# Kernel optimization log

Hardware: AMD Instinct MI355X
Metric: run time of the kernel (lower is better)

The kernel has to match this reference:

```python
import jax, jax.numpy as jnp
import numpy as np

D_MODEL = 1024
NUM_HEADS = 16
D_K = D_MODEL // NUM_HEADS


def setup_inputs() -> dict:
    key = jax.random.key(0)
    ks = jax.random.split(key, 12)
    B, S = 2, 2048
    s = 1.0 / np.sqrt(D_MODEL)
    inp = {
        "query": jax.random.normal(ks[0], (B, S, D_MODEL), jnp.float32),
        "key": jax.random.normal(ks[1], (B, S, D_MODEL), jnp.float32),
        "value": jax.random.normal(ks[2], (B, S, D_MODEL), jnp.float32),
        "w_q": jax.random.normal(ks[3], (D_MODEL, D_MODEL), jnp.float32) * s,
        "b_q": jax.random.normal(ks[4], (D_MODEL,), jnp.float32) * 0.01,
        "w_k": jax.random.normal(ks[5], (D_MODEL, D_MODEL), jnp.float32) * s,
        "b_k": jax.random.normal(ks[6], (D_MODEL,), jnp.float32) * 0.01,
        "w_v": jax.random.normal(ks[7], (D_MODEL, D_MODEL), jnp.float32) * s,
        "b_v": jax.random.normal(ks[8], (D_MODEL,), jnp.float32) * 0.01,
        "w_o": jax.random.normal(ks[9], (D_MODEL, D_MODEL), jnp.float32) * s,
        "b_o": jax.random.normal(ks[10], (D_MODEL,), jnp.float32) * 0.01,
    }
    return inp


def _split_heads(x):
    # [B, S, d_model] -> [B, H, S, d_k]
    B, S, _ = x.shape
    return x.reshape(B, S, NUM_HEADS, D_K).transpose(0, 2, 1, 3)


def reference(query, key, value, w_q, b_q, w_k, b_k, w_v, b_v, w_o, b_o):
    B, S, _ = query.shape
    Q = _split_heads(query @ w_q.T + b_q)
    K = _split_heads(key @ w_k.T + b_k)
    V = _split_heads(value @ w_v.T + b_v)
    scale = 1.0 / jnp.sqrt(jnp.asarray(D_K, Q.dtype))
    scores = jnp.einsum("bhqd,bhkd->bhqk", Q, K) * scale  # [B,H,S,S]
    attn = jax.nn.softmax(scores, axis=-1)
    ctx = jnp.einsum("bhqk,bhkd->bhqd", attn, V)
    ctx = ctx.transpose(0, 2, 1, 3).reshape(B, S, D_MODEL)
    return ctx @ w_o.T + b_o
```

## Files before the change

kernel.cpp:

```cpp
#include <hip/hip_runtime.h>
#include <hip/hip_bf16.h>
#include <stdint.h>

#define D_MODEL 1024
#define NHEAD   16
#define DK      64
#define SEQ     2048
#define BATCH   2

using bf16 = __bf16;
typedef __bf16 bf16x8 __attribute__((ext_vector_type(8)));
typedef float  f32x4  __attribute__((ext_vector_type(4)));
typedef float  f32x16 __attribute__((ext_vector_type(16)));
typedef unsigned uintx2 __attribute__((ext_vector_type(2)));

__device__ __forceinline__ unsigned short f2bf(float x) {
  return __builtin_bit_cast(unsigned short, (__bf16)x);
}
__device__ __forceinline__ unsigned pk2bf(float a, float b) {
  return (unsigned)f2bf(a) | ((unsigned)f2bf(b) << 16);
}
__device__ __forceinline__ float uasf(unsigned x) {
  return __builtin_bit_cast(float, x);
}
__device__ __forceinline__ unsigned fasu(float x) {
  return __builtin_bit_cast(unsigned, x);
}

__device__ __forceinline__ void gld_lds16(const void* g, void* l) {
  __builtin_amdgcn_global_load_lds(
      (const __attribute__((address_space(1))) void*)g,
      (__attribute__((address_space(3))) void*)l, 16, 0, 0);
}

__device__ __forceinline__ float xhalf_sum(float x) {
  uintx2 r = __builtin_amdgcn_permlane32_swap(fasu(x), fasu(x), false, false);
  return uasf(r[0]) + uasf(r[1]);
}

#define MHA_PACK(sv, off, dst)                                           \
  {                                                                      \
    float e0 = __builtin_amdgcn_exp2f(sv[off + 0]);                      \
    float e1 = __builtin_amdgcn_exp2f(sv[off + 1]);                      \
    float e2 = __builtin_amdgcn_exp2f(sv[off + 2]);                      \
    float e3 = __builtin_amdgcn_exp2f(sv[off + 3]);                      \
    float e4 = __builtin_amdgcn_exp2f(sv[off + 4]);                      \
    float e5 = __builtin_amdgcn_exp2f(sv[off + 5]);                      \
    float e6 = __builtin_amdgcn_exp2f(sv[off + 6]);                      \
    float e7 = __builtin_amdgcn_exp2f(sv[off + 7]);                      \
    ps += ((e0 + e1) + (e2 + e3)) + ((e4 + e5) + (e6 + e7));             \
    unsigned c0 = pk2bf(e0, e1), c1 = pk2bf(e2, e3);                     \
    unsigned c2 = pk2bf(e4, e5), c3 = pk2bf(e6, e7);                     \
    uintx2 r02 = __builtin_amdgcn_permlane32_swap(c0, c2, false, false); \
    uintx2 r13 = __builtin_amdgcn_permlane32_swap(c1, c3, false, false); \
    uint4 w; w.x = r02[0]; w.y = r13[0]; w.z = r02[1]; w.w = r13[1];     \
    dst = __builtin_bit_cast(bf16x8, w);                                 \
  }

struct ConvArgs {
  const float* src[7];
  bf16* dst[7];
};

__global__ __launch_bounds__(256) void convert_f32_bf16(ConvArgs a) {
  int v = blockIdx.x * 256 + threadIdx.x;
  int seg, off;
  if (v < 3 * 1048576) { seg = v >> 20; off = v & (1048576 - 1); }
  else { int u = v - 3 * 1048576; seg = 3 + (u >> 18); off = u & (262144 - 1); }
  float4 f = ((const float4*)a.src[seg])[off];
  ushort4 o;
  o.x = f2bf(f.x); o.y = f2bf(f.y); o.z = f2bf(f.z); o.w = f2bf(f.w);
  ((ushort4*)a.dst[seg])[off] = o;
}

__device__ __forceinline__ void gemm_qkv_core(
    const bf16* __restrict__ A, const bf16* __restrict__ B,
    const float* __restrict__ bias, bf16* __restrict__ Cout,
    int mode, int bx, int by, float oscale, char* lds) {
  constexpr int BUF = 16384;
  constexpr int NKT = D_MODEL / 32;
  const int tid  = threadIdx.x;
  const int lane = tid & 63;
  const int wave = tid >> 6;
  const int wr = wave >> 1, wc = wave & 1;
  const int t = lane >> 4, q = lane & 15;

  f32x4 acc[4][4];
#pragma unroll
  for (int i = 0; i < 4; ++i)
#pragma unroll
    for (int j = 0; j < 4; ++j) acc[i][j] = (f32x4){0.f, 0.f, 0.f, 0.f};

  const char* Abase = (const char*)(A + (size_t)bx * 128 * D_MODEL);
  const char* Bbase = (const char*)(B + (size_t)by * 128 * D_MODEL);

  const char* gA[2]; char* sA[2]; const char* gB[2]; char* sB[2];
#pragma unroll
  for (int i = 0; i < 2; ++i) {
    int c = tid + i * 256, row = c >> 2;
    int src = ((c & 3) * 16) ^ ((row & 3) << 4);
    gA[i] = Abase + (size_t)row * (D_MODEL * 2) + src;
    sA[i] = lds + c * 16;
    gB[i] = Bbase + (size_t)row * (D_MODEL * 2) + src;
    sB[i] = lds + 8192 + c * 16;
  }

  const char* aA[4]; const char* aB[4];
#pragma unroll
  for (int f = 0; f < 4; ++f) {
    int ra = wr * 64 + f * 16 + q;
    aA[f] = lds + ra * 64 + ((t * 16) ^ ((q & 3) << 4));
    int rb = wc * 64 + f * 16 + q;
    aB[f] = lds + 8192 + rb * 64 + ((t * 16) ^ ((q & 3) << 4));
  }

#pragma unroll
  for (int i = 0; i < 2; ++i) { gld_lds16(gA[i], sA[i]); gld_lds16(gB[i], sB[i]); }
#pragma unroll
  for (int i = 0; i < 2; ++i) {
    gld_lds16(gA[i] + 64, sA[i] + BUF); gld_lds16(gB[i] + 64, sB[i] + BUF);
  }
  asm volatile("s_waitcnt vmcnt(4)" ::: "memory");
  __builtin_amdgcn_s_barrier();

#pragma unroll
  for (int kt = 0; kt < NKT; ++kt) {
    const int CUR = (kt % 3) * BUF;
    if (kt + 2 < NKT) {
      const int NB = ((kt + 2) % 3) * BUF;
#pragma unroll
      for (int i = 0; i < 2; ++i) {
        gld_lds16(gA[i] + (kt + 2) * 64, sA[i] + NB);
        gld_lds16(gB[i] + (kt + 2) * 64, sB[i] + NB);
      }
    }
    bf16x8 af[4], bfv[4];
#pragma unroll
    for (int f = 0; f < 4; ++f) af[f]  = *(const bf16x8*)(aA[f] + CUR);
#pragma unroll
    for (int f = 0; f < 4; ++f) bfv[f] = *(const bf16x8*)(aB[f] + CUR);
    __builtin_amdgcn_s_setprio(1);
#pragma unroll
    for (int fm = 0; fm < 4; ++fm)
#pragma unroll
      for (int fn = 0; fn < 4; ++fn)
        acc[fm][fn] = __builtin_amdgcn_mfma_f32_16x16x32_bf16(
            af[fm], bfv[fn], acc[fm][fn], 0, 0, 0);
    __builtin_amdgcn_s_setprio(0);
    if (kt + 2 < NKT)      asm volatile("s_waitcnt vmcnt(4)" ::: "memory");
    else if (kt + 1 < NKT) asm volatile("s_waitcnt vmcnt(0)" ::: "memory");
    __builtin_amdgcn_s_barrier();
  }

#pragma unroll
  for (int fm = 0; fm < 4; ++fm)
#pragma unroll
    for (int fn = 0; fn < 4; ++fn)
#pragma unroll
      for (int jj = 0; jj < 4; ++jj) {
        int m = bx * 128 + wr * 64 + fm * 16 + t * 4 + jj;
        int n = by * 128 + wc * 64 + fn * 16 + q;
        float v = acc[fm][fn][jj];
        if (mode == 0) {
          v = (v + bias[n]) * oscale;
          int b = m >> 11, s = m & (SEQ - 1), h = n >> 6, d = n & 63;
          Cout[(((size_t)(b * NHEAD + h)) * SEQ + s) * DK + d] = (bf16)v;
        } else {
          v += bias[m];
          int h = m >> 6, d = m & 63, b = n >> 11, s = n & (SEQ - 1);
          Cout[(((size_t)(b * NHEAD + h)) * DK + d) * SEQ + s] = (bf16)v;
        }
      }
}

struct QkvArgs {
  const bf16* A[3]; const bf16* B[3]; const float* bias[3]; bf16* out[3];
};

__global__ __launch_bounds__(256, 2) void gemm_qkv(QkvArgs a) {
  __shared__ char lds[3 * 16384];
  int z = blockIdx.z;
  int mode = (z == 2) ? 1 : 0;
  int bx = (z == 2) ? blockIdx.y : blockIdx.x;
  int by = (z == 2) ? blockIdx.x : blockIdx.y;
  float osc = (z == 0) ? 0.18033688011112042f : 1.0f;
  gemm_qkv_core(a.A[z], a.B[z], a.bias[z], a.out[z], mode, bx, by, osc, lds);
}

template <int BM>
__device__ __forceinline__ void gemm_core(
    const bf16* __restrict__ A, const bf16* __restrict__ B,
    const float* __restrict__ bias, float* __restrict__ Cout,
    int bx, int by, char* lds) {
  constexpr int FM   = BM / 32;
  constexpr int ACH  = BM / 32;
  constexpr int HALF = BM * 128 + 16384;
  const int tid  = threadIdx.x;
  const int lane = tid & 63;
  const int wave = tid >> 6;
  const int wr = wave >> 1, wc = wave & 1;
  const int t = lane >> 4, q = lane & 15;

  f32x4 acc[FM][4];
#pragma unroll
  for (int i = 0; i < FM; ++i)
#pragma unroll
    for (int j = 0; j < 4; ++j) acc[i][j] = (f32x4){0.f, 0.f, 0.f, 0.f};

  const char* Abase = (const char*)(A + (size_t)bx * BM * D_MODEL);
  const char* Bbase = (const char*)(B + (size_t)by * 128 * D_MODEL);

  const char* gA[ACH]; char* sA[ACH];
  const char* gB[4];   char* sB[4];
#pragma unroll
  for (int i = 0; i < ACH; ++i) {
    int c = tid + i * 256, row = c >> 3;
    int src = ((c & 7) * 16) ^ ((row & 7) << 4);
    gA[i] = Abase + (size_t)row * (D_MODEL * 2) + src;
    sA[i] = lds + c * 16;
  }
#pragma unroll
  for (int i = 0; i < 4; ++i) {
    int c = tid + i * 256, row = c >> 3;
    int src = ((c & 7) * 16) ^ ((row & 7) << 4);
    gB[i] = Bbase + (size_t)row * (D_MODEL * 2) + src;
    sB[i] = lds + BM * 128 + c * 16;
  }

  const char* aA[FM][2]; const char* aB[4][2];
#pragma unroll
  for (int f = 0; f < FM; ++f)
#pragma unroll
    for (int ks = 0; ks < 2; ++ks) {
      int ra = wr * (BM / 2) + f * 16 + q;
      aA[f][ks] = lds + ra * 128 + ((ks * 64 + t * 16) ^ ((q & 7) << 4));
    }
#pragma unroll
  for (int f = 0; f < 4; ++f)
#pragma unroll
    for (int ks = 0; ks < 2; ++ks) {
      int rb = wc * 64 + f * 16 + q;
      aB[f][ks] = lds + BM * 128 + rb * 128 + ((ks * 64 + t * 16) ^ ((q & 7) << 4));
    }

#pragma unroll
  for (int i = 0; i < ACH; ++i) gld_lds16(gA[i], sA[i]);
#pragma unroll
  for (int i = 0; i < 4; ++i)  gld_lds16(gB[i], sB[i]);
  __syncthreads();

  auto ktile = [&](int kt, int CUR) {
    if (kt + 1 < D_MODEL / 64) {
      int NXT = CUR ^ HALF;
#pragma unroll
      for (int i = 0; i < ACH; ++i) gld_lds16(gA[i] + (kt + 1) * 128, sA[i] + NXT);
#pragma unroll
      for (int i = 0; i < 4; ++i)  gld_lds16(gB[i] + (kt + 1) * 128, sB[i] + NXT);
    }
#pragma unroll
    for (int ks = 0; ks < 2; ++ks) {
      bf16x8 af[FM], bfv[4];
#pragma unroll
      for (int f = 0; f < FM; ++f) af[f] = *(const bf16x8*)(aA[f][ks] + CUR);
#pragma unroll
      for (int f = 0; f < 4; ++f)  bfv[f] = *(const bf16x8*)(aB[f][ks] + CUR);
      __builtin_amdgcn_s_setprio(1);
#pragma unroll
      for (int fm = 0; fm < FM; ++fm)
#pragma unroll
        for (int fn = 0; fn < 4; ++fn)
          acc[fm][fn] = __builtin_amdgcn_mfma_f32_16x16x32_bf16(
              af[fm], bfv[fn], acc[fm][fn], 0, 0, 0);
      __builtin_amdgcn_s_setprio(0);
    }
    __syncthreads();
  };
  for (int kt = 0; kt < D_MODEL / 64; kt += 2) {
    ktile(kt, 0);
    ktile(kt + 1, HALF);
  }

#pragma unroll
  for (int fm = 0; fm < FM; ++fm)
#pragma unroll
    for (int fn = 0; fn < 4; ++fn)
#pragma unroll
      for (int jj = 0; jj < 4; ++jj) {
        int m = bx * BM + wr * (BM / 2) + fm * 16 + t * 4 + jj;
        int n = by * 128 + wc * 64 + fn * 16 + q;
        Cout[(size_t)m * D_MODEL + n] = acc[fm][fn][jj] + bias[n];
      }
}

__global__ __launch_bounds__(256, 2) void gemm_o(
    const bf16* __restrict__ A, const bf16* __restrict__ B,
    const float* __restrict__ bias, float* __restrict__ Cout) {
  __shared__ char lds[2 * (64 * 128 + 16384)];
  gemm_core<64>(A, B, bias, Cout, blockIdx.x, blockIdx.y, lds);
}

__global__ __launch_bounds__(512, 2) void flash_attn(
    const bf16* __restrict__ Qh, const bf16* __restrict__ Kh,
    const bf16* __restrict__ Vt, bf16* __restrict__ ctx) {
  __shared__ char lds[65536];
  const int tid  = threadIdx.x;
  const int lane = tid & 63;
  const int wave = tid >> 6;
  const int lo = lane & 31;
  const int hi = lane >> 5;
  const int grp = wave >> 2;
  const int wq  = wave & 3;
  const int bh = blockIdx.x;
  const int q0 = blockIdx.y * 128 + wq * 32;

  const bf16* Qb = Qh + (size_t)bh * SEQ * DK;
  const char* Kb = (const char*)(Kh + (size_t)bh * SEQ * DK) + grp * 1024 * 128;
  const char* Vb = (const char*)(Vt + (size_t)bh * DK * SEQ) + grp * 1024 * 2;
  char* Kg = lds + grp * 16384;
  char* Vg = lds + 32768 + grp * 16384;

  bf16x8 qf[4];
#pragma unroll
  for (int c = 0; c < 4; ++c)
    qf[c] = *(const bf16x8*)(Qb + (size_t)(q0 + lo) * DK + c * 16 + hi * 8);

  const int tg = tid & 255;
  const int srow = tg >> 3;
  const int ssrc = ((tg & 7) * 16) ^ ((srow & 7) << 4);
  const char* gK0 = Kb + (size_t)srow * 128 + ssrc;
  const char* gK1 = Kb + (size_t)(srow + 32) * 128 + ssrc;
  const char* gV0 = Vb + (size_t)srow * 4096 + ssrc;
  const char* gV1 = Vb + (size_t)(srow + 32) * 4096 + ssrc;
  char* sK0 = Kg + tg * 16;
  char* sK1 = Kg + 4096 + tg * 16;
  char* sV0 = Vg + tg * 16;
  char* sV1 = Vg + 4096 + tg * 16;

  const int key = (lo & 7) << 4;
  const char* KA[4]; const char* VA[4];
#pragma unroll
  for (int c = 0; c < 4; ++c) {
    int o = (((2 * c + hi) * 16) ^ key) + lo * 128;
    KA[c] = Kg + o;
    VA[c] = Vg + o;
  }

  f32x16 acc0 = {}, acc1 = {};
  float lsum = 0.f;

  gld_lds16(gK0, sK0); gld_lds16(gK1, sK1);
  gld_lds16(gV0, sV0); gld_lds16(gV1, sV1);
  __syncthreads();

  auto tile = [&](int kt, int CUR) {
    if (kt + 1 < 16) {
      int nb = CUR ^ 8192;
      gld_lds16(gK0 + (kt + 1) * 8192, sK0 + nb);
      gld_lds16(gK1 + (kt + 1) * 8192, sK1 + nb);
      gld_lds16(gV0 + (kt + 1) * 128,  sV0 + nb);
      gld_lds16(gV1 + (kt + 1) * 128,  sV1 + nb);
    }

    float ps = 0.f;
    bf16x8 pa[4];

    {
      bf16x8 kf0[4], kf1[4];
#pragma unroll
      for (int c = 0; c < 4; ++c) {
        kf0[c] = *(const bf16x8*)(KA[c] + CUR);
        kf1[c] = *(const bf16x8*)(KA[c] + CUR + 4096);
      }
      f32x16 s0 = {}, s1 = {};
      __builtin_amdgcn_s_setprio(1);
#pragma unroll
      for (int c = 0; c < 4; ++c) {
        s0 = __builtin_amdgcn_mfma_f32_32x32x16_bf16(kf0[c], qf[c], s0, 0, 0, 0);
        s1 = __builtin_amdgcn_mfma_f32_32x32x16_bf16(kf1[c], qf[c], s1, 0, 0, 0);
      }
      __builtin_amdgcn_s_setprio(0);
      MHA_PACK(s0, 0, pa[0]);
      MHA_PACK(s0, 8, pa[1]);
      MHA_PACK(s1, 0, pa[2]);
      MHA_PACK(s1, 8, pa[3]);
    }
    lsum += ps;

    bf16x8 vf[2][4];
#pragma unroll
    for (int ks = 0; ks < 4; ++ks) {
      vf[0][ks] = *(const bf16x8*)(VA[ks] + CUR);
      vf[1][ks] = *(const bf16x8*)(VA[ks] + CUR + 4096);
    }
    __builtin_amdgcn_s_setprio(1);
#pragma unroll
    for (int ks = 0; ks < 4; ++ks) {
      acc0 = __builtin_amdgcn_mfma_f32_32x32x16_bf16(pa[ks], vf[0][ks], acc0, 0, 0, 0);
      acc1 = __builtin_amdgcn_mfma_f32_32x32x16_bf16(pa[ks], vf[1][ks], acc1, 0, 0, 0);
    }
    __builtin_amdgcn_s_setprio(0);

    __syncthreads();
  };

  for (int kt = 0; kt < 16; kt += 2) {
    tile(kt, 0);
    tile(kt + 1, 8192);
  }

  float lrun = xhalf_sum(lsum);

  float* lsh = (float*)lds;
  float* U1  = (float*)(lds + 4096);
  if (hi == 0) lsh[grp * 128 + wq * 32 + lo] = lrun;
  if (grp == 1) {
    float* dst = U1 + (size_t)(wq * 64 + lane) * 33;
#pragma unroll
    for (int r = 0; r < 16; ++r) { dst[r] = acc0[r]; dst[16 + r] = acc1[r]; }
  }
  __syncthreads();
  if (grp == 0) {
    const float* src = U1 + (size_t)(wq * 64 + lane) * 33;
    int b = bh >> 4, h = bh & 15;
#pragma unroll
    for (int r = 0; r < 16; ++r) {
      int row = (r & 3) + 8 * (r >> 2) + 4 * hi;
      int gr = wq * 32 + row;
      float linv = 1.f / (lsh[gr] + lsh[128 + gr]);
      float o0 = (acc0[r] + src[r]) * linv;
      float o1 = (acc1[r] + src[16 + r]) * linv;
      int srw = q0 + row;
      size_t base = ((size_t)(b * SEQ + srw)) * D_MODEL + h * 64 + lo;
      ctx[base]      = (bf16)o0;
      ctx[base + 32] = (bf16)o1;
    }
  }
}

extern "C" void kernel_launch(void* const* d_in, const int* in_sizes, int n_in,
                              void* d_out, int out_size, void* d_ws, size_t ws_size,
                              hipStream_t stream) {
  const float* query = (const float*)d_in[0];
  const float* key_  = (const float*)d_in[1];
  const float* value = (const float*)d_in[2];
  const float* w_q = (const float*)d_in[3];
  const float* b_q = (const float*)d_in[4];
  const float* w_k = (const float*)d_in[5];
  const float* b_k = (const float*)d_in[6];
  const float* w_v = (const float*)d_in[7];
  const float* b_v = (const float*)d_in[8];
  const float* w_o = (const float*)d_in[9];
  const float* b_o = (const float*)d_in[10];

  char* ws = (char*)d_ws;
  const size_t MB = 1024 * 1024;
  bf16* bQ  = (bf16*)(ws + 0 * MB);
  bf16* bK  = (bf16*)(ws + 8 * MB);
  bf16* bV  = (bf16*)(ws + 16 * MB);
  bf16* bWq = (bf16*)(ws + 24 * MB);
  bf16* bWk = (bf16*)(ws + 26 * MB);
  bf16* bWv = (bf16*)(ws + 28 * MB);
  bf16* bWo = (bf16*)(ws + 30 * MB);
  bf16* Qh  = (bf16*)(ws + 32 * MB);
  bf16* Kh  = (bf16*)(ws + 40 * MB);
  bf16* Vth = (bf16*)(ws + 48 * MB);
  bf16* ctx = (bf16*)(ws + 56 * MB);

  ConvArgs ca;
  ca.src[0] = query; ca.src[1] = key_; ca.src[2] = value;
  ca.src[3] = w_q;   ca.src[4] = w_k;  ca.src[5] = w_v; ca.src[6] = w_o;
  ca.dst[0] = bQ;  ca.dst[1] = bK;  ca.dst[2] = bV;
  ca.dst[3] = bWq; ca.dst[4] = bWk; ca.dst[5] = bWv; ca.dst[6] = bWo;
  convert_f32_bf16<<<16384, 256, 0, stream>>>(ca);

  QkvArgs qa;
  qa.A[0] = bQ;  qa.B[0] = bWq; qa.bias[0] = b_q; qa.out[0] = Qh;
  qa.A[1] = bK;  qa.B[1] = bWk; qa.bias[1] = b_k; qa.out[1] = Kh;
  qa.A[2] = bWv; qa.B[2] = bV;  qa.bias[2] = b_v; qa.out[2] = Vth;
  gemm_qkv<<<dim3(32, 8, 3), 256, 0, stream>>>(qa);

  flash_attn<<<dim3(32, 16), 512, 0, stream>>>(Qh, Kh, Vth, ctx);

  gemm_o<<<dim3(64, 8), 256, 0, stream>>>(ctx, bWo, b_o, (float*)d_out);
}
```

Measured before the change: 125.4 us.

## Double per-wave query rows in flash attention to reuse K/V tiles

Each wave now handles 64 query rows instead of 32, so every block covers 256 queries and the grid shrinks from 512 to 256 blocks. Each K and V fragment loaded from LDS now feeds twice as many MFMAs, which halves total K/V global and LDS traffic per query. In exchange, register pressure roughly doubles (launch bounds relaxed to one block per CU), occupancy and grid parallelism drop, and the epilogue reduction runs in two passes with extra barriers.

```diff
diff --git a/kernel.cpp b/kernel.cpp
--- a/kernel.cpp
+++ b/kernel.cpp
@@ -299,7 +299,7 @@
   gemm_core<64>(A, B, bias, Cout, blockIdx.x, blockIdx.y, lds);
 }
 
-__global__ __launch_bounds__(512, 2) void flash_attn(
+__global__ __launch_bounds__(512, 1) void flash_attn(
     const bf16* __restrict__ Qh, const bf16* __restrict__ Kh,
     const bf16* __restrict__ Vt, bf16* __restrict__ ctx) {
   __shared__ char lds[65536];
@@ -311,7 +311,7 @@
   const int grp = wave >> 2;
   const int wq  = wave & 3;
   const int bh = blockIdx.x;
-  const int q0 = blockIdx.y * 128 + wq * 32;
+  const int q0 = blockIdx.y * 256 + wq * 64;
 
   const bf16* Qb = Qh + (size_t)bh * SEQ * DK;
   const char* Kb = (const char*)(Kh + (size_t)bh * SEQ * DK) + grp * 1024 * 128;
@@ -319,10 +319,12 @@
   char* Kg = lds + grp * 16384;
   char* Vg = lds + 32768 + grp * 16384;
 
-  bf16x8 qf[4];
-#pragma unroll
-  for (int c = 0; c < 4; ++c)
-    qf[c] = *(const bf16x8*)(Qb + (size_t)(q0 + lo) * DK + c * 16 + hi * 8);
+  bf16x8 qf0[4], qf1[4];
+#pragma unroll
+  for (int c = 0; c < 4; ++c) {
+    qf0[c] = *(const bf16x8*)(Qb + (size_t)(q0 + lo) * DK + c * 16 + hi * 8);
+    qf1[c] = *(const bf16x8*)(Qb + (size_t)(q0 + 32 + lo) * DK + c * 16 + hi * 8);
+  }
 
   const int tg = tid & 255;
   const int srow = tg >> 3;
@@ -345,8 +347,8 @@
     VA[c] = Vg + o;
   }
 
-  f32x16 acc0 = {}, acc1 = {};
-  float lsum = 0.f;
+  f32x16 acc00 = {}, acc01 = {}, acc10 = {}, acc11 = {};
+  float lsum0 = 0.f, lsum1 = 0.f;
 
   gld_lds16(gK0, sK0); gld_lds16(gK1, sK1);
   gld_lds16(gV0, sV0); gld_lds16(gV1, sV1);
@@ -361,9 +363,7 @@
       gld_lds16(gV1 + (kt + 1) * 128,  sV1 + nb);
     }
 
-    float ps = 0.f;
-    bf16x8 pa[4];
-
+    bf16x8 pa0[4], pa1[4];
     {
       bf16x8 kf0[4], kf1[4];
 #pragma unroll
@@ -371,20 +371,29 @@
         kf0[c] = *(const bf16x8*)(KA[c] + CUR);
         kf1[c] = *(const bf16x8*)(KA[c] + CUR + 4096);
       }
-      f32x16 s0 = {}, s1 = {};
+      f32x16 s00 = {}, s01 = {}, s10 = {}, s11 = {};
       __builtin_amdgcn_s_setprio(1);
 #pragma unroll
       for (int c = 0; c < 4; ++c) {
-        s0 = __builtin_amdgcn_mfma_f32_32x32x16_bf16(kf0[c], qf[c], s0, 0, 0, 0);
-        s1 = __builtin_amdgcn_mfma_f32_32x32x16_bf16(kf1[c], qf[c], s1, 0, 0, 0);
+        s00 = __builtin_amdgcn_mfma_f32_32x32x16_bf16(kf0[c], qf0[c], s00, 0, 0, 0);
+        s01 = __builtin_amdgcn_mfma_f32_32x32x16_bf16(kf0[c], qf1[c], s01, 0, 0, 0);
+        s10 = __builtin_amdgcn_mfma_f32_32x32x16_bf16(kf1[c], qf0[c], s10, 0, 0, 0);
+        s11 = __builtin_amdgcn_mfma_f32_32x32x16_bf16(kf1[c], qf1[c], s11, 0, 0, 0);
       }
       __builtin_amdgcn_s_setprio(0);
-      MHA_PACK(s0, 0, pa[0]);
-      MHA_PACK(s0, 8, pa[1]);
-      MHA_PACK(s1, 0, pa[2]);
-      MHA_PACK(s1, 8, pa[3]);
-    }
-    lsum += ps;
+      float ps = 0.f;
+      MHA_PACK(s00, 0, pa0[0]);
+      MHA_PACK(s00, 8, pa0[1]);
+      MHA_PACK(s10, 0, pa0[2]);
+      MHA_PACK(s10, 8, pa0[3]);
+      lsum0 += ps;
+      ps = 0.f;
+      MHA_PACK(s01, 0, pa1[0]);
+      MHA_PACK(s01, 8, pa1[1]);
+      MHA_PACK(s11, 0, pa1[2]);
+      MHA_PACK(s11, 8, pa1[3]);
+      lsum1 += ps;
+    }
 
     bf16x8 vf[2][4];
 #pragma unroll
@@ -395,8 +404,10 @@
     __builtin_amdgcn_s_setprio(1);
 #pragma unroll
     for (int ks = 0; ks < 4; ++ks) {
-      acc0 = __builtin_amdgcn_mfma_f32_32x32x16_bf16(pa[ks], vf[0][ks], acc0, 0, 0, 0);
-      acc1 = __builtin_amdgcn_mfma_f32_32x32x16_bf16(pa[ks], vf[1][ks], acc1, 0, 0, 0);
+      acc00 = __builtin_amdgcn_mfma_f32_32x32x16_bf16(pa0[ks], vf[0][ks], acc00, 0, 0, 0);
+      acc01 = __builtin_amdgcn_mfma_f32_32x32x16_bf16(pa0[ks], vf[1][ks], acc01, 0, 0, 0);
+      acc10 = __builtin_amdgcn_mfma_f32_32x32x16_bf16(pa1[ks], vf[0][ks], acc10, 0, 0, 0);
+      acc11 = __builtin_amdgcn_mfma_f32_32x32x16_bf16(pa1[ks], vf[1][ks], acc11, 0, 0, 0);
     }
     __builtin_amdgcn_s_setprio(0);
 
@@ -408,31 +419,41 @@
     tile(kt + 1, 8192);
   }
 
-  float lrun = xhalf_sum(lsum);
+  float lrun0 = xhalf_sum(lsum0);
+  float lrun1 = xhalf_sum(lsum1);
 
   float* lsh = (float*)lds;
   float* U1  = (float*)(lds + 4096);
-  if (hi == 0) lsh[grp * 128 + wq * 32 + lo] = lrun;
-  if (grp == 1) {
-    float* dst = U1 + (size_t)(wq * 64 + lane) * 33;
-#pragma unroll
-    for (int r = 0; r < 16; ++r) { dst[r] = acc0[r]; dst[16 + r] = acc1[r]; }
-  }
-  __syncthreads();
-  if (grp == 0) {
-    const float* src = U1 + (size_t)(wq * 64 + lane) * 33;
-    int b = bh >> 4, h = bh & 15;
-#pragma unroll
-    for (int r = 0; r < 16; ++r) {
-      int row = (r & 3) + 8 * (r >> 2) + 4 * hi;
-      int gr = wq * 32 + row;
-      float linv = 1.f / (lsh[gr] + lsh[128 + gr]);
-      float o0 = (acc0[r] + src[r]) * linv;
-      float o1 = (acc1[r] + src[16 + r]) * linv;
-      int srw = q0 + row;
-      size_t base = ((size_t)(b * SEQ + srw)) * D_MODEL + h * 64 + lo;
-      ctx[base]      = (bf16)o0;
-      ctx[base + 32] = (bf16)o1;
+  if (hi == 0) {
+    lsh[grp * 256 + wq * 64 + lo]      = lrun0;
+    lsh[grp * 256 + wq * 64 + 32 + lo] = lrun1;
+  }
+  int b = bh >> 4, h = bh & 15;
+#pragma unroll
+  for (int qb = 0; qb < 2; ++qb) {
+    const f32x16& a0 = qb ? acc10 : acc00;
+    const f32x16& a1 = qb ? acc11 : acc01;
+    __syncthreads();
+    if (grp == 1) {
+      float* dst = U1 + (size_t)(wq * 64 + lane) * 33;
+#pragma unroll
+      for (int r = 0; r < 16; ++r) { dst[r] = a0[r]; dst[16 + r] = a1[r]; }
+    }
+    __syncthreads();
+    if (grp == 0) {
+      const float* src = U1 + (size_t)(wq * 64 + lane) * 33;
+#pragma unroll
+      for (int r = 0; r < 16; ++r) {
+        int row = (r & 3) + 8 * (r >> 2) + 4 * hi;
+        int gr = wq * 64 + qb * 32 + row;
+        float linv = 1.f / (lsh[gr] + lsh[256 + gr]);
+        float o0 = (a0[r] + src[r]) * linv;
+        float o1 = (a1[r] + src[16 + r]) * linv;
+        int srw = q0 + qb * 32 + row;
+        size_t base = ((size_t)(b * SEQ + srw)) * D_MODEL + h * 64 + lo;
+        ctx[base]      = (bf16)o0;
+        ctx[base + 32] = (bf16)o1;
+      }
     }
   }
 }
@@ -479,7 +500,7 @@
   qa.A[2] = bWv; qa.B[2] = bV;  qa.bias[2] = b_v; qa.out[2] = Vth;
   gemm_qkv<<<dim3(32, 8, 3), 256, 0, stream>>>(qa);
 
-  flash_attn<<<dim3(32, 16), 512, 0, stream>>>(Qh, Kh, Vth, ctx);
+  flash_attn<<<dim3(32, 8), 512, 0, stream>>>(Qh, Kh, Vth, ctx);
 
   gemm_o<<<dim3(64, 8), 256, 0, stream>>>(ctx, bWo, b_o, (float*)d_out);
 }
```

Result: faster. 122.8 us, median of 4 (-2.1%).
